# Performance work log

Measured on AMD Instinct MI355X. Metric: run time of the kernel, lower is better.

The kernel has to match this reference:

```python
import jax, jax.numpy as jnp
import numpy as np

D_MODEL = 1024
N_HEADS = 16
D_HEAD = D_MODEL // N_HEADS
D_FF = 4096
B, T = 2, 2048
EPS = 1e-6


def setup_inputs() -> dict:
    key = jax.random.key(0)
    ks = jax.random.split(key, 10)
    s = 0.02
    return {
        "x": jax.random.normal(ks[0], (B, T, D_MODEL), dtype=jnp.float32),
        # Linear weights stored as (in, out) so y = x @ W (equivalent to torch x @ W.T)
        "Wq": jax.random.normal(ks[1], (D_MODEL, D_MODEL), dtype=jnp.float32) * s,
        "Wk": jax.random.normal(ks[2], (D_MODEL, D_MODEL), dtype=jnp.float32) * s,
        "Wv": jax.random.normal(ks[3], (D_MODEL, D_MODEL), dtype=jnp.float32) * s,
        "Wo": jax.random.normal(ks[4], (D_MODEL, D_MODEL), dtype=jnp.float32) * s,
        "W1": jax.random.normal(ks[5], (D_MODEL, D_FF), dtype=jnp.float32) * s,
        "b1": jnp.zeros((D_FF,), dtype=jnp.float32),
        "W2": jax.random.normal(ks[6], (D_FF, D_MODEL), dtype=jnp.float32) * s,
        "b2": jnp.zeros((D_MODEL,), dtype=jnp.float32),
        "g1": jnp.ones((D_MODEL,), dtype=jnp.float32),
        "g2": jnp.ones((D_MODEL,), dtype=jnp.float32),
    }


def rmsnorm(x, g):
    return x * jax.lax.rsqrt(jnp.mean(x * x, axis=-1, keepdims=True) + EPS) * g


def attention(x, Wq, Wk, Wv, Wo):
    b, t, c = x.shape
    def split_heads(y):  # [B,T,C] -> [B,H,T,Dh]
        return y.reshape(b, t, N_HEADS, D_HEAD).transpose(0, 2, 1, 3)
    q = split_heads(x @ Wq)
    k = split_heads(x @ Wk)
    v = split_heads(x @ Wv)
    att = jnp.einsum("bhqd,bhkd->bhqk", q, k) / jnp.sqrt(jnp.float32(D_HEAD))
    causal = jnp.tril(jnp.ones((t, t), dtype=bool))
    att = jnp.where(causal[None, None], att, -jnp.inf)
    att = jax.nn.softmax(att, axis=-1)
    y = jnp.einsum("bhqk,bhkd->bhqd", att, v)
    y = y.transpose(0, 2, 1, 3).reshape(b, t, c)
    return y @ Wo


def reference(x, Wq, Wk, Wv, Wo, W1, b1, W2, b2, g1, g2):
    x = x + attention(rmsnorm(x, g1), Wq, Wk, Wv, Wo)
    h = rmsnorm(x, g2)
    h = jax.nn.gelu(h @ W1 + b1, approximate=False) @ W2 + b2
    return x + h
```

## Files before the change

kernel.cpp:

```cpp
#include <hip/hip_runtime.h>
#include <hip/hip_bf16.h>
#include <math.h>
#include <stdint.h>


typedef __bf16 v8bf  __attribute__((ext_vector_type(8)));
typedef float  v4f   __attribute__((ext_vector_type(4)));

#define T_SEQ 2048
#define EXP2F(x) __builtin_amdgcn_exp2f(x)

#define FRAG(base, R, ko) \
  (*(const v8bf*)((base) + (R) * 64 + (((((ko) >> 3) ^ ((R) & 7))) << 3)))

__device__ __forceinline__ void async_ld16(const void* g, void* l) {
  __builtin_amdgcn_global_load_lds(
      (const __attribute__((address_space(1))) uint32_t*)g,
      (__attribute__((address_space(3))) uint32_t*)l, 16, 0, 0);
}

__global__ __launch_bounds__(256) void transpose_w4(
    const float* __restrict__ Wq, const float* __restrict__ Wk,
    const float* __restrict__ Wv, const float* __restrict__ Wo,
    __hip_bfloat16* __restrict__ out)
{
  __shared__ float tile[32][33];
  const int z = blockIdx.z;
  const float* W = z == 0 ? Wq : z == 1 ? Wk : z == 2 ? Wv : Wo;
  const int n0 = blockIdx.x * 32, k0 = blockIdx.y * 32;
  const int tx = threadIdx.x, ty = threadIdx.y;
#pragma unroll
  for (int i = 0; i < 32; i += 8)
    tile[ty + i][tx] = W[(size_t)(k0 + ty + i) * 1024 + n0 + tx];
  __syncthreads();
  __hip_bfloat16* o = out + (size_t)z * 1024 * 1024;
#pragma unroll
  for (int i = 0; i < 32; i += 8)
    o[(size_t)(n0 + ty + i) * 1024 + k0 + tx] = __float2bfloat16(tile[tx][ty + i]);
}

__global__ __launch_bounds__(256) void transpose_w(
    const float* __restrict__ W, __hip_bfloat16* __restrict__ WT,
    int K, int N, int ldo)
{
  __shared__ float tile[32][33];
  const int n0 = blockIdx.x * 32, k0 = blockIdx.y * 32;
  const int tx = threadIdx.x, ty = threadIdx.y;
#pragma unroll
  for (int i = 0; i < 32; i += 8)
    tile[ty + i][tx] = W[(size_t)(k0 + ty + i) * N + n0 + tx];
  __syncthreads();
#pragma unroll
  for (int i = 0; i < 32; i += 8)
    WT[(size_t)(n0 + ty + i) * ldo + k0 + tx] = __float2bfloat16(tile[tx][ty + i]);
}

__global__ __launch_bounds__(256) void transpose_v(
    const __hip_bfloat16* __restrict__ QKV, __hip_bfloat16* __restrict__ VTg)
{
  __shared__ float tile[32][33];
  const int t0 = blockIdx.x * 32;
  const int bh = blockIdx.y >> 1;
  const int dt = (blockIdx.y & 1) * 32;
  const int b = bh >> 4, h = bh & 15;
  const int tx = threadIdx.x, ty = threadIdx.y;
#pragma unroll
  for (int i = 0; i < 32; i += 8)
    tile[ty + i][tx] = __bfloat162float(
        QKV[(size_t)(b * T_SEQ + t0 + ty + i) * 3072 + 2048 + h * 64 + dt + tx]);
  __syncthreads();
#pragma unroll
  for (int i = 0; i < 32; i += 8)
    VTg[((size_t)bh * 64 + dt + ty + i) * T_SEQ + t0 + tx] =
        __float2bfloat16(tile[tx][ty + i]);
}

__global__ __launch_bounds__(256) void rmsnorm_kernel(
    const float* __restrict__ x, const float* __restrict__ g,
    __hip_bfloat16* __restrict__ out,
    const float* __restrict__ bias, float* __restrict__ dinit)
{
  const int row = blockIdx.x;
  const int t = threadIdx.x;
  const float4 v = ((const float4*)(x + (size_t)row * 1024))[t];
  float ss = v.x * v.x + v.y * v.y + v.z * v.z + v.w * v.w;
#pragma unroll
  for (int off = 32; off; off >>= 1) ss += __shfl_xor(ss, off, 64);
  __shared__ float red[4];
  if ((t & 63) == 0) red[t >> 6] = ss;
  __syncthreads();
  ss = red[0] + red[1] + red[2] + red[3];
  const float rs = rsqrtf(ss * (1.0f / 1024.0f) + 1e-6f);
  const float4 gv = ((const float4*)g)[t];
  __hip_bfloat16* o = out + (size_t)row * 1024 + t * 4;
  o[0] = __float2bfloat16(v.x * rs * gv.x);
  o[1] = __float2bfloat16(v.y * rs * gv.y);
  o[2] = __float2bfloat16(v.z * rs * gv.z);
  o[3] = __float2bfloat16(v.w * rs * gv.w);
  if (dinit) {
    const float4 bv = ((const float4*)bias)[t];
    float4 d;
    d.x = v.x + bv.x; d.y = v.y + bv.y; d.z = v.z + bv.z; d.w = v.w + bv.w;
    ((float4*)(dinit + (size_t)row * 1024))[t] = d;
  }
}

template <int MODE, int MT, int PX, int PY>
__global__ __launch_bounds__(256, 2) void gemm_bt(
    const __hip_bfloat16* __restrict__ A,
    const __hip_bfloat16* __restrict__ BT,
    const float* __restrict__ bias,
    const float* __restrict__ resid,
    __hip_bfloat16* __restrict__ outb,
    float* __restrict__ outf,
    int M, int N, int K, int Ksub)
{
  __shared__ __align__(16) __hip_bfloat16 As[32 * MT * 64];
  __shared__ __align__(16) __hip_bfloat16 Bs[128 * 64];
  const int tid = threadIdx.x;
  const int wave = tid >> 6, lane = tid & 63;
  const int quad = lane >> 4, l16 = lane & 15;

  int bx = blockIdx.x, by = blockIdx.y;
  {
    const int id = by * gridDim.x + bx;
    const int k = id & 7, s = id >> 3;
    const int pw = gridDim.x / PX, ph = gridDim.y / PY;
    bx = (k % PX) * pw + (s % pw);
    by = (k / PX) * ph + (s / pw);
  }
  const int m0 = by * (32 * MT), n0 = bx * 128;
  const size_t kb = (size_t)blockIdx.z * Ksub;
  const int wr = (wave >> 1) * (16 * MT), wc = (wave & 1) * 64;
  const int lrow = lane >> 3;
  const int scol = ((lane & 7) ^ lrow) * 8;

  v4f acc[MT][4];
#pragma unroll
  for (int i = 0; i < MT; i++)
#pragma unroll
    for (int j = 0; j < 4; j++)
#pragma unroll
      for (int c = 0; c < 4; c++) acc[i][j][c] = 0.0f;

  for (int k0 = 0; k0 < Ksub; k0 += 64) {
#pragma unroll
    for (int i = 0; i < MT + 4; i++) {
      const int c = wave * (MT + 4) + i;
      if (c < 4 * MT) {
        async_ld16(A + (size_t)(m0 + c * 8 + lrow) * K + kb + k0 + scol, As + c * 512);
      } else {
        const int cb = c - 4 * MT;
        async_ld16(BT + (size_t)(n0 + cb * 8 + lrow) * K + kb + k0 + scol,
                   Bs + cb * 512);
      }
    }
    __syncthreads();
#pragma unroll
    for (int ks = 0; ks < 64; ks += 32) {
      v8bf af[MT], bf[4];
#pragma unroll
      for (int mt = 0; mt < MT; mt++)
        af[mt] = FRAG(As, wr + mt * 16 + l16, ks + quad * 8);
#pragma unroll
      for (int nt = 0; nt < 4; nt++)
        bf[nt] = FRAG(Bs, wc + nt * 16 + l16, ks + quad * 8);
#pragma unroll
      for (int mt = 0; mt < MT; mt++)
#pragma unroll
        for (int nt = 0; nt < 4; nt++)
          acc[mt][nt] = __builtin_amdgcn_mfma_f32_16x16x32_bf16(
              af[mt], bf[nt], acc[mt][nt], 0, 0, 0);
    }
    __syncthreads();
  }

#pragma unroll
  for (int mt = 0; mt < MT; mt++) {
#pragma unroll
    for (int r = 0; r < 4; r++) {
      const int gm = m0 + wr + mt * 16 + quad * 4 + r;
#pragma unroll
      for (int nt = 0; nt < 4; nt++) {
        const int gn = n0 + wc + nt * 16 + l16;
        float v = acc[mt][nt][r];
        if (MODE == 0) {
          outb[(size_t)gm * N + gn] = __float2bfloat16(v);
        } else if (MODE == 1) {
          outf[(size_t)gm * N + gn] = resid[(size_t)gm * N + gn] + v;
        } else if (MODE == 2) {
          v += bias[gn];
          const float u = 0.7978845608f * (v + 0.044715f * v * v * v);
          const float e = EXP2F(u * 2.885390082f);
          const float th = 1.0f - 2.0f * __builtin_amdgcn_rcpf(e + 1.0f);
          v = 0.5f * v * (1.0f + th);
          outb[(size_t)gm * N + gn] = __float2bfloat16(v);
        } else {
          atomicAdd(&outf[(size_t)gm * N + gn], v);
        }
      }
    }
  }
}

__global__ __launch_bounds__(256, 2) void attn_kernel(
    const __hip_bfloat16* __restrict__ QKV,
    const __hip_bfloat16* __restrict__ VTg,
    __hip_bfloat16* __restrict__ Y)
{
  __shared__ __align__(16) __hip_bfloat16 Ks[2 * 64 * 64];
  __shared__ __align__(16) __hip_bfloat16 Vs[2 * 64 * 64];
  __shared__ __align__(16) __hip_bfloat16 PsA[64 * 64];
  __shared__ __align__(16) __hip_bfloat16 PsB[64 * 64];

  const int tid = threadIdx.x;
  const int wave = tid >> 6, lane = tid & 63;
  const int quad = lane >> 4, l16 = lane & 15;
  const int blk = blockIdx.x;
  const int p = blk & 15, h = (blk >> 4) & 15, b = blk >> 8;
  const int qa = p, qb = 31 - p, kmax = qb;
  const size_t rowbase = (size_t)b * T_SEQ;
  const size_t vbase = (size_t)(b * 16 + h) * 64;
  const int lrow = lane >> 3, scol = ((lane & 7) ^ (lane >> 3)) * 8;

  const float QSC = 0.125f * 1.44269504f;
  v8bf aqA[2], aqB[2];
#pragma unroll
  for (int ks = 0; ks < 2; ks++) {
    v8bf q = *(const v8bf*)(QKV + (rowbase + qa * 64 + wave * 16 + l16) * 3072 +
                            h * 64 + ks * 32 + quad * 8);
#pragma unroll
    for (int j = 0; j < 8; j++) aqA[ks][j] = (__bf16)((float)q[j] * QSC);
    q = *(const v8bf*)(QKV + (rowbase + qb * 64 + wave * 16 + l16) * 3072 +
                       h * 64 + ks * 32 + quad * 8);
#pragma unroll
    for (int j = 0; j < 8; j++) aqB[ks][j] = (__bf16)((float)q[j] * QSC);
  }

  v4f oA[4], oB[4];
  float lpA[4], lpB[4];
#pragma unroll
  for (int i = 0; i < 4; i++) {
    lpA[i] = 0.0f; lpB[i] = 0.0f;
#pragma unroll
    for (int c = 0; c < 4; c++) { oA[i][c] = 0.0f; oB[i][c] = 0.0f; }
  }

  auto stage = [&](int kt, int buf) {
#pragma unroll
    for (int i = 0; i < 2; i++) {
      const int r8 = i * 32 + wave * 8;
      const int rr = r8 + lrow;
      async_ld16(QKV + (rowbase + kt * 64 + rr) * 3072 + 1024 + h * 64 + scol,
                 Ks + buf * 4096 + r8 * 64);
      async_ld16(VTg + (vbase + rr) * T_SEQ + kt * 64 + scol,
                 Vs + buf * 4096 + r8 * 64);
    }
  };
  stage(0, 0);

  auto softmax_store = [&](v4f s[4], float lp[4], __hip_bfloat16* Ps, bool diag) {
    if (diag) {
#pragma unroll
      for (int nt = 0; nt < 4; nt++) {
        const int colr = nt * 16 + l16;
#pragma unroll
        for (int r = 0; r < 4; r++)
          if (colr > wave * 16 + quad * 4 + r) s[nt][r] = -30000.0f;
      }
    }
#pragma unroll
    for (int r = 0; r < 4; r++) {
      const int row = wave * 16 + quad * 4 + r;
      const int rsw = (quad * 4 + r) & 7;
#pragma unroll
      for (int nt = 0; nt < 4; nt++) {
        const float e = EXP2F(s[nt][r]);
        lp[r] += e;
        const int chunk = (nt * 2 + (l16 >> 3)) ^ rsw;
        Ps[row * 64 + (chunk << 3) + (l16 & 7)] = __float2bfloat16(e);
      }
    }
  };

  for (int kt = 0; kt <= kmax; kt++) {
    __syncthreads();
    if (kt < kmax) stage(kt + 1, (kt + 1) & 1);
    const __hip_bfloat16* Kb = Ks + (kt & 1) * 4096;
    const __hip_bfloat16* Vb = Vs + (kt & 1) * 4096;
    const bool doA = (kt <= qa);

    {
      v8bf kf[2][4];
#pragma unroll
      for (int ks = 0; ks < 2; ks++)
#pragma unroll
        for (int nt = 0; nt < 4; nt++)
          kf[ks][nt] = FRAG(Kb, nt * 16 + l16, ks * 32 + quad * 8);

      v4f sB[4];
#pragma unroll
      for (int nt = 0; nt < 4; nt++)
#pragma unroll
        for (int c = 0; c < 4; c++) sB[nt][c] = 0.0f;
#pragma unroll
      for (int ks = 0; ks < 2; ks++)
#pragma unroll
        for (int nt = 0; nt < 4; nt++)
          sB[nt] = __builtin_amdgcn_mfma_f32_16x16x32_bf16(aqB[ks], kf[ks][nt],
                                                           sB[nt], 0, 0, 0);
      softmax_store(sB, lpB, PsB, kt == qb);

      if (doA) {
        v4f sA[4];
#pragma unroll
        for (int nt = 0; nt < 4; nt++)
#pragma unroll
          for (int c = 0; c < 4; c++) sA[nt][c] = 0.0f;
#pragma unroll
        for (int ks = 0; ks < 2; ks++)
#pragma unroll
          for (int nt = 0; nt < 4; nt++)
            sA[nt] = __builtin_amdgcn_mfma_f32_16x16x32_bf16(aqA[ks], kf[ks][nt],
                                                             sA[nt], 0, 0, 0);
        softmax_store(sA, lpA, PsA, kt == qa);
      }
    }

    {
      v8bf vf[2][4];
#pragma unroll
      for (int ks = 0; ks < 2; ks++)
#pragma unroll
        for (int nt = 0; nt < 4; nt++)
          vf[ks][nt] = FRAG(Vb, nt * 16 + l16, ks * 32 + quad * 8);
#pragma unroll
      for (int ks = 0; ks < 2; ks++) {
        const v8bf apB = FRAG(PsB, wave * 16 + l16, ks * 32 + quad * 8);
#pragma unroll
        for (int nt = 0; nt < 4; nt++)
          oB[nt] = __builtin_amdgcn_mfma_f32_16x16x32_bf16(apB, vf[ks][nt],
                                                           oB[nt], 0, 0, 0);
      }
      if (doA) {
#pragma unroll
        for (int ks = 0; ks < 2; ks++) {
          const v8bf apA = FRAG(PsA, wave * 16 + l16, ks * 32 + quad * 8);
#pragma unroll
          for (int nt = 0; nt < 4; nt++)
            oA[nt] = __builtin_amdgcn_mfma_f32_16x16x32_bf16(apA, vf[ks][nt],
                                                             oA[nt], 0, 0, 0);
        }
      }
    }
  }

#pragma unroll
  for (int r = 0; r < 4; r++) {
    float la = lpA[r], lb = lpB[r];
#pragma unroll
    for (int off = 1; off < 16; off <<= 1) {
      la += __shfl_xor(la, off, 16);
      lb += __shfl_xor(lb, off, 16);
    }
    const float ila = 1.0f / la, ilb = 1.0f / lb;
#pragma unroll
    for (int nt = 0; nt < 4; nt++) {
      Y[(rowbase + qa * 64 + wave * 16 + quad * 4 + r) * 1024 + h * 64 + nt * 16 + l16] =
          __float2bfloat16(oA[nt][r] * ila);
      Y[(rowbase + qb * 64 + wave * 16 + quad * 4 + r) * 1024 + h * 64 + nt * 16 + l16] =
          __float2bfloat16(oB[nt][r] * ilb);
    }
  }
}

extern "C" void kernel_launch(void* const* d_in, const int* in_sizes, int n_in,
                              void* d_out, int out_size, void* d_ws, size_t ws_size,
                              hipStream_t stream)
{
  const float* x  = (const float*)d_in[0];
  const float* Wq = (const float*)d_in[1];
  const float* Wk = (const float*)d_in[2];
  const float* Wv = (const float*)d_in[3];
  const float* Wo = (const float*)d_in[4];
  const float* W1 = (const float*)d_in[5];
  const float* b1 = (const float*)d_in[6];
  const float* W2 = (const float*)d_in[7];
  const float* b2 = (const float*)d_in[8];
  const float* g1 = (const float*)d_in[9];
  const float* g2 = (const float*)d_in[10];

  uint8_t* ws = (uint8_t*)d_ws;
  __hip_bfloat16* WqkvT = (__hip_bfloat16*)(ws + 0);
  __hip_bfloat16* WoT   = (__hip_bfloat16*)(ws + 6291456);
  __hip_bfloat16* W1T   = (__hip_bfloat16*)(ws + 8388608);
  __hip_bfloat16* W2T   = (__hip_bfloat16*)(ws + 16777216);
  float*          x1    = (float*)(ws + 25165824);
  __hip_bfloat16* xn    = (__hip_bfloat16*)(ws + 41943040);
  __hip_bfloat16* Ybuf  = (__hip_bfloat16*)(ws + 41943040);
  __hip_bfloat16* QKV   = (__hip_bfloat16*)(ws + 50331648);
  __hip_bfloat16* VTg   = (__hip_bfloat16*)(ws + 75497472);
  __hip_bfloat16* Hbuf  = (__hip_bfloat16*)(ws + 50331648);

  const dim3 tb(32, 8);
  transpose_w4<<<dim3(32, 32, 4), tb, 0, stream>>>(Wq, Wk, Wv, Wo, WqkvT);
  transpose_w<<<dim3(128, 32), tb, 0, stream>>>(W1, W1T, 1024, 4096, 1024);
  transpose_w<<<dim3(32, 128), tb, 0, stream>>>(W2, W2T, 4096, 1024, 4096);

  rmsnorm_kernel<<<4096, 256, 0, stream>>>(x, g1, xn, nullptr, nullptr);
  gemm_bt<0, 4, 4, 2><<<dim3(24, 32), 256, 0, stream>>>(
      xn, WqkvT, nullptr, nullptr, QKV, nullptr, 4096, 3072, 1024, 1024);
  transpose_v<<<dim3(64, 64), tb, 0, stream>>>(QKV, VTg);
  attn_kernel<<<512, 256, 0, stream>>>(QKV, VTg, Ybuf);
  gemm_bt<1, 2, 1, 8><<<dim3(8, 64), 256, 0, stream>>>(
      Ybuf, WoT, nullptr, x, nullptr, x1, 4096, 1024, 1024, 1024);
  rmsnorm_kernel<<<4096, 256, 0, stream>>>(x1, g2, xn, b2, (float*)d_out);
  gemm_bt<2, 4, 4, 2><<<dim3(32, 32), 256, 0, stream>>>(
      xn, W1T, b1, nullptr, Hbuf, nullptr, 4096, 4096, 1024, 1024);
  gemm_bt<4, 2, 1, 8><<<dim3(8, 64, 2), 256, 0, stream>>>(
      Hbuf, W2T, nullptr, nullptr, nullptr, (float*)d_out, 4096, 1024, 4096, 2048);
}
```

Baseline: 329.8 us.

## Add 256x256-tile pipelined GEMM kernel for QKV, FFN1 and FFN2

Adds a new 512-thread GEMM with 256x256 output tiles, double-buffered async global-to-LDS loads interleaved with MFMA quarters, and s_setprio around the MFMA bursts. It replaces the older 128-tile gemm_bt for the QKV projection, the W1 GELU GEMM and the split-K W2 GEMM, the last now using 4-way split-K with atomics. The larger tiles raise data reuse per LDS load and let loads overlap compute. In exchange they lower the block count, and with it occupancy and tail balance, and the extra split-K partitions add more atomic traffic.

```diff
diff --git a/kernel.cpp b/kernel.cpp
--- a/kernel.cpp
+++ b/kernel.cpp
@@ -17,6 +17,12 @@
   __builtin_amdgcn_global_load_lds(
       (const __attribute__((address_space(1))) uint32_t*)g,
       (__attribute__((address_space(3))) uint32_t*)l, 16, 0, 0);
+}
+
+__device__ __forceinline__ void wg_barrier() {
+  asm volatile("" ::: "memory");
+  __builtin_amdgcn_s_barrier();
+  asm volatile("" ::: "memory");
 }
 
 __global__ __launch_bounds__(256) void transpose_w4(
@@ -158,19 +164,19 @@
     __syncthreads();
 #pragma unroll
     for (int ks = 0; ks < 64; ks += 32) {
-      v8bf af[MT], bf[4];
+      v8bf af[MT], bfr[4];
 #pragma unroll
       for (int mt = 0; mt < MT; mt++)
         af[mt] = FRAG(As, wr + mt * 16 + l16, ks + quad * 8);
 #pragma unroll
       for (int nt = 0; nt < 4; nt++)
-        bf[nt] = FRAG(Bs, wc + nt * 16 + l16, ks + quad * 8);
+        bfr[nt] = FRAG(Bs, wc + nt * 16 + l16, ks + quad * 8);
 #pragma unroll
       for (int mt = 0; mt < MT; mt++)
 #pragma unroll
         for (int nt = 0; nt < 4; nt++)
           acc[mt][nt] = __builtin_amdgcn_mfma_f32_16x16x32_bf16(
-              af[mt], bf[nt], acc[mt][nt], 0, 0, 0);
+              af[mt], bfr[nt], acc[mt][nt], 0, 0, 0);
     }
     __syncthreads();
   }
@@ -203,6 +209,154 @@
   }
 }
 
+template <int MODE, int PX, int PY>
+__global__ __launch_bounds__(512, 2) void gemm256(
+    const __hip_bfloat16* __restrict__ A,
+    const __hip_bfloat16* __restrict__ BT,
+    const float* __restrict__ bias,
+    __hip_bfloat16* __restrict__ outb,
+    float* __restrict__ outf,
+    int M, int N, int K, int Ksub)
+{
+  __shared__ __align__(16) __hip_bfloat16 As[2 * 256 * 64];
+  __shared__ __align__(16) __hip_bfloat16 Bs[2 * 256 * 64];
+  (void)M;
+  const int tid = threadIdx.x;
+  const int wave = tid >> 6, lane = tid & 63;
+  const int quad = lane >> 4, l16 = lane & 15;
+  const int wm = wave >> 2, wn = wave & 3;
+  const int lrow = lane >> 3, scol = ((lane & 7) ^ lrow) * 8;
+
+  int bx = blockIdx.x, by = blockIdx.y;
+  {
+    const int id = by * gridDim.x + bx;
+    const int k = id & 7, s = id >> 3;
+    const int pw = gridDim.x / PX, ph = gridDim.y / PY;
+    bx = (k % PX) * pw + (s % pw);
+    by = (k / PX) * ph + (s / pw);
+  }
+  const int m0 = by * 256, n0 = bx * 256;
+  const size_t kb = (size_t)blockIdx.z * Ksub;
+  const int NT = Ksub >> 6;
+  const int cg = wave * 2;
+
+  auto stageA = [&](int h, int tt) {
+#pragma unroll
+    for (int j = 0; j < 2; j++) {
+      const int rg = cg + j;
+      async_ld16(A + (size_t)(m0 + h * 128 + rg * 8 + lrow) * K + kb + tt * 64 + scol,
+                 As + ((tt & 1) * 16384 + (h * 128 + rg * 8) * 64));
+    }
+  };
+  auto stageB = [&](int h, int tt) {
+#pragma unroll
+    for (int j = 0; j < 2; j++) {
+      const int rg = cg + j;
+      async_ld16(BT + (size_t)(n0 + h * 128 + rg * 8 + lrow) * K + kb + tt * 64 + scol,
+                 Bs + ((tt & 1) * 16384 + (h * 128 + rg * 8) * 64));
+    }
+  };
+
+  v4f acc[8][4];
+#pragma unroll
+  for (int i = 0; i < 8; i++)
+#pragma unroll
+    for (int j = 0; j < 4; j++)
+#pragma unroll
+      for (int c = 0; c < 4; c++) acc[i][j][c] = 0.0f;
+
+  stageA(0, 0); stageB(0, 0); stageB(1, 0); stageA(1, 0);
+  if (NT > 1) {
+    stageA(0, 1); stageB(1, 1);
+    asm volatile("s_waitcnt vmcnt(4)" ::: "memory");
+  } else {
+    asm volatile("s_waitcnt vmcnt(0)" ::: "memory");
+  }
+  wg_barrier();
+
+#define READ_A(mh)                                                          \
+  _Pragma("unroll") for (int mt = 0; mt < 4; mt++)                          \
+      _Pragma("unroll") for (int ks = 0; ks < 2; ks++)                      \
+          af[mt][ks] =                                                      \
+              FRAG(Ab, (mh) * 128 + wm * 64 + mt * 16 + l16, ks * 32 + quad * 8)
+#define READ_B(dst, nh)                                                     \
+  _Pragma("unroll") for (int nt = 0; nt < 2; nt++)                          \
+      _Pragma("unroll") for (int ks = 0; ks < 2; ks++)                      \
+          dst[nt][ks] =                                                     \
+              FRAG(Bb, (nh) * 128 + wn * 32 + nt * 16 + l16, ks * 32 + quad * 8)
+#define MM16(mh, bsrc, nh)                                                  \
+  __builtin_amdgcn_s_setprio(1);                                            \
+  _Pragma("unroll") for (int mt = 0; mt < 4; mt++)                          \
+      _Pragma("unroll") for (int nt = 0; nt < 2; nt++)                      \
+          _Pragma("unroll") for (int ks = 0; ks < 2; ks++)                  \
+              acc[(mh) * 4 + mt][(nh) * 2 + nt] =                           \
+                  __builtin_amdgcn_mfma_f32_16x16x32_bf16(                  \
+                      af[mt][ks], bsrc[nt][ks],                             \
+                      acc[(mh) * 4 + mt][(nh) * 2 + nt], 0, 0, 0);          \
+  __builtin_amdgcn_s_setprio(0)
+
+  for (int t = 0; t < NT; ++t) {
+    const __hip_bfloat16* Ab = As + (t & 1) * 16384;
+    const __hip_bfloat16* Bb = Bs + (t & 1) * 16384;
+    v8bf af[4][2], b0[2][2], b1[2][2];
+    READ_A(0); READ_B(b0, 0);
+    if (t + 1 < NT) stageA(1, t + 1);
+    wg_barrier();
+    MM16(0, b0, 0);
+    wg_barrier();
+    READ_B(b1, 1);
+    if (t + 1 < NT) stageB(0, t + 1);
+    wg_barrier();
+    MM16(0, b1, 1);
+    wg_barrier();
+    READ_A(1);
+    if (t + 2 < NT) stageA(0, t + 2);
+    wg_barrier();
+    MM16(1, b1, 1);
+    wg_barrier();
+    if (t + 2 < NT) stageB(1, t + 2);
+    wg_barrier();
+    MM16(1, b0, 0);
+    if (t + 2 < NT) {
+      asm volatile("s_waitcnt vmcnt(4)" ::: "memory");
+    } else if (t + 1 < NT) {
+      asm volatile("s_waitcnt vmcnt(0)" ::: "memory");
+    }
+    wg_barrier();
+  }
+#undef READ_A
+#undef READ_B
+#undef MM16
+
+#pragma unroll
+  for (int ni = 0; ni < 4; ni++) {
+    const int gn = n0 + (ni >> 1) * 128 + wn * 32 + (ni & 1) * 16 + l16;
+    float bcol = 0.0f;
+    if (MODE == 2) bcol = bias[gn];
+#pragma unroll
+    for (int mi = 0; mi < 8; mi++) {
+      const int gmb = m0 + (mi >> 2) * 128 + wm * 64 + (mi & 3) * 16 + quad * 4;
+#pragma unroll
+      for (int r = 0; r < 4; r++) {
+        float v = acc[mi][ni][r];
+        const size_t idx = (size_t)(gmb + r) * N + gn;
+        if (MODE == 0) {
+          outb[idx] = __float2bfloat16(v);
+        } else if (MODE == 2) {
+          v += bcol;
+          const float u = 0.7978845608f * (v + 0.044715f * v * v * v);
+          const float e = EXP2F(u * 2.885390082f);
+          const float th = 1.0f - 2.0f * __builtin_amdgcn_rcpf(e + 1.0f);
+          v = 0.5f * v * (1.0f + th);
+          outb[idx] = __float2bfloat16(v);
+        } else {
+          atomicAdd(&outf[idx], v);
+        }
+      }
+    }
+  }
+}
+
 __global__ __launch_bounds__(256, 2) void attn_kernel(
     const __hip_bfloat16* __restrict__ QKV,
     const __hip_bfloat16* __restrict__ VTg,
@@ -408,15 +562,15 @@
   transpose_w<<<dim3(32, 128), tb, 0, stream>>>(W2, W2T, 4096, 1024, 4096);
 
   rmsnorm_kernel<<<4096, 256, 0, stream>>>(x, g1, xn, nullptr, nullptr);
-  gemm_bt<0, 4, 4, 2><<<dim3(24, 32), 256, 0, stream>>>(
-      xn, WqkvT, nullptr, nullptr, QKV, nullptr, 4096, 3072, 1024, 1024);
+  gemm256<0, 4, 2><<<dim3(12, 16), 512, 0, stream>>>(
+      xn, WqkvT, nullptr, QKV, nullptr, 4096, 3072, 1024, 1024);
   transpose_v<<<dim3(64, 64), tb, 0, stream>>>(QKV, VTg);
   attn_kernel<<<512, 256, 0, stream>>>(QKV, VTg, Ybuf);
   gemm_bt<1, 2, 1, 8><<<dim3(8, 64), 256, 0, stream>>>(
       Ybuf, WoT, nullptr, x, nullptr, x1, 4096, 1024, 1024, 1024);
   rmsnorm_kernel<<<4096, 256, 0, stream>>>(x1, g2, xn, b2, (float*)d_out);
-  gemm_bt<2, 4, 4, 2><<<dim3(32, 32), 256, 0, stream>>>(
-      xn, W1T, b1, nullptr, Hbuf, nullptr, 4096, 4096, 1024, 1024);
-  gemm_bt<4, 2, 1, 8><<<dim3(8, 64, 2), 256, 0, stream>>>(
-      Hbuf, W2T, nullptr, nullptr, nullptr, (float*)d_out, 4096, 1024, 4096, 2048);
-}
+  gemm256<2, 4, 2><<<dim3(16, 16), 512, 0, stream>>>(
+      xn, W1T, b1, Hbuf, nullptr, 4096, 4096, 1024, 1024);
+  gemm256<4, 4, 2><<<dim3(4, 16, 4), 512, 0, stream>>>(
+      Hbuf, W2T, nullptr, nullptr, (float*)d_out, 4096, 1024, 4096, 1024);
+}
```

Measured after the change: 353.0 us. 1.07x slower.
